# Kernel optimization log

Hardware: AMD Instinct MI355X
Metric: run time of the kernel (lower is better)

Reference implementation:

```python
import jax, jax.numpy as jnp
import numpy as np

GELU = lambda v: jax.nn.gelu(v, approximate=False)  # torch nn.GELU default (exact erf)


def _gconv(x, w):
    # grouped conv1d, valid padding; w: (C,1,K), groups=C. lax conv = cross-correlation, same as torch.
    return jax.lax.conv_general_dilated(x, w, (1,), [(0, 0)],
                                        dimension_numbers=('NCH', 'OIH', 'NCH'),
                                        feature_group_count=x.shape[1])


def _conv(x, w, b):
    # dense conv1d, kernel 3, padding=1
    y = jax.lax.conv_general_dilated(x, w, (1,), [(1, 1)],
                                     dimension_numbers=('NCH', 'OIH', 'NCH'))
    return y + b[None, :, None]


def setup_inputs() -> dict:
    key = jax.random.key(0)
    ks = jax.random.split(key, 12)
    B, C, L = 8, 64, 2048
    H, FL, HD, TD, level = 32, 8, 64, 16, 3
    Cs = (1 + level) * C  # 256 channels into the ODE
    n = lambda k, s: (jax.random.normal(k, s) * 0.05).astype(jnp.float32)
    z = lambda s: jnp.zeros(s, jnp.float32)
    return dict(
        x=jax.random.normal(ks[0], (B, C, L), jnp.float32),
        # DyWAN_QR params
        sw1=n(ks[1], (H, C)), sb1=z((H,)),
        sw2=n(ks[2], (H, H)), sb2=z((H,)),
        sw3=n(ks[3], (2 * FL, H)), sb3=z((2 * FL,)),
        # ODE time embed / FiLM params
        tw1=n(ks[4], (TD, 1)), tb1=z((TD,)),
        tw2=n(ks[5], (TD, TD)), tb2=z((TD,)),
        cw=n(ks[6], (2 * HD, TD)), cb=z((2 * HD,)),
        # ODE conv stack params
        k1=n(ks[7], (HD, Cs, 3)), kb1=z((HD,)),
        k2=n(ks[8], (HD, HD, 3)), kb2=z((HD,)),
        k3=n(ks[9], (Cs, HD, 3)), kb3=z((Cs,)),
    )


def reference(x, sw1, sb1, sw2, sb2, sw3, sb3, tw1, tb1, tw2, tb2, cw, cb,
              k1, kb1, k2, kb2, k3, kb3):
    B, C, L = x.shape
    level, FL, T = 3, 8, 5

    def dywan(a):
        # stat_net: adaptive max pool over L -> (B,C) -> Linear -> GELU
        feat = GELU(jnp.max(a, axis=-1) @ sw1.T + sb1)
        raw = GELU(feat @ sw2.T + sb2) @ sw3.T + sb3  # (B, 2*FL)
        lo_raw, hi_raw = raw[:, :FL], raw[:, FL:]
        # QR of an (FL,1) column vector == L2 normalization (up to LAPACK sign)
        lo = lo_raw / jnp.linalg.norm(lo_raw, axis=1, keepdims=True)
        hi = hi_raw / jnp.linalg.norm(hi_raw, axis=1, keepdims=True)
        return lo, hi

    pad = FL - 1
    coeffs = [x]
    approx = x
    for _ in range(level):
        lo, hi = dywan(approx)
        lo_f = jnp.broadcast_to(lo.mean(0)[None, None, :], (C, 1, FL))
        hi_f = jnp.broadcast_to(hi.mean(0)[None, None, :], (C, 1, FL))
        ap = jnp.pad(approx, ((0, 0), (0, 0), (pad // 2, pad - pad // 2)), mode='reflect')
        new_approx = _gconv(ap, lo_f)[..., :L]
        coeffs.append(_gconv(ap, hi_f)[..., :L])
        approx = new_approx
    stacked = jnp.concatenate(coeffs, axis=1)  # (B, (1+level)*C, L)

    def ode_f(t, y):
        te = jnp.reshape(t, (1, 1)).astype(y.dtype)
        te = GELU(te @ tw1.T + tb1) @ tw2.T + tb2          # (1, TD)
        cond = te @ cw.T + cb                               # (1, 2*HD)
        hd = cond.shape[1] // 2
        gamma, beta = cond[:, :hd], cond[:, hd:]
        h = _conv(y, k1, kb1)
        h = (1.0 + gamma[:, :, None]) * h + beta[:, :, None]  # FiLM
        h = GELU(h)
        h = GELU(_conv(h, k2, kb2))
        return _conv(h, k3, kb3)

    # dopri5 tableau, fixed grid over linspace(0, 1, T) (b7 = 0, so 6 stages)
    hs = 1.0 / (T - 1)
    y = stacked
    for i in range(T - 1):
        t0 = i * hs
        s1 = ode_f(t0, y)
        s2 = ode_f(t0 + hs / 5, y + hs * (1 / 5) * s1)
        s3 = ode_f(t0 + 3 * hs / 10, y + hs * (3 / 40 * s1 + 9 / 40 * s2))
        s4 = ode_f(t0 + 4 * hs / 5, y + hs * (44 / 45 * s1 - 56 / 15 * s2 + 32 / 9 * s3))
        s5 = ode_f(t0 + 8 * hs / 9, y + hs * (19372 / 6561 * s1 - 25360 / 2187 * s2
                                              + 64448 / 6561 * s3 - 212 / 729 * s4))
        s6 = ode_f(t0 + hs, y + hs * (9017 / 3168 * s1 - 355 / 33 * s2 + 46732 / 5247 * s3
                                      + 49 / 176 * s4 - 5103 / 18656 * s5))
        y = y + hs * (35 / 384 * s1 + 500 / 1113 * s3 + 125 / 192 * s4
                      - 2187 / 6784 * s5 + 11 / 84 * s6)
    ode_out = y

    yl = ode_out[:, :C, :]
    yh0 = ode_out[:, C:2 * C, :]
    yh1 = ode_out[:, 2 * C:3 * C, :]
    yh2 = ode_out[:, 3 * C:4 * C, :]

    dx = ode_f(jnp.float32(1.0), ode_out)
    inner = jnp.sum(stacked * dx, axis=(1, 2))  # (B,)
    ecloss = jnp.mean(inner ** 2)
    return (yl, yh0, yh1, yh2, ecloss)
```

## Files before the change

kernel.cpp:

```cpp
#include <hip/hip_runtime.h>
#include <math.h>

#define B 8
#define C 64
#define L 2048
#define CS 256
#define BCL  (B*C*L)
#define BCSL (B*CS*L)
#define HS 0.25f

typedef unsigned short u16;
typedef unsigned int   u32;
typedef __attribute__((ext_vector_type(8))) short sh8;
typedef __attribute__((ext_vector_type(4))) float f4;
typedef __attribute__((ext_vector_type(8))) unsigned short us8;
typedef __attribute__((ext_vector_type(4))) unsigned short us4;

__device__ __forceinline__ float gelu(float x) {
    return 0.5f * x * (1.0f + erff(x * 0.70710678118654752440f));
}
__device__ __forceinline__ u16 f2b(float f) {
    u32 u = __float_as_uint(f);
    u32 r = u + 0x7FFFu + ((u >> 16) & 1u);
    return (u16)(r >> 16);
}
__device__ __forceinline__ float b2f(u16 h) {
    return __uint_as_float(((u32)h) << 16);
}

struct ComboB { const u16* p[6]; float c[6]; };

__global__ __launch_bounds__(256) void prep_k(const float* __restrict__ w,
        u16* __restrict__ dst, int IC, int OC) {
    int idx = blockIdx.x * 256 + threadIdx.x;
    int OCG = OC >> 4;
    int j = idx & 7, lane = (idx >> 3) & 63, t = idx >> 9;
    int ocg = t % OCG, c = t / OCG;
    int oc = ocg * 16 + (lane & 15);
    int K = c * 32 + ((lane >> 4) & 3) * 8 + j;
    int kk = K / IC, ic = K % IC;
    dst[idx] = f2b(w[((size_t)oc * IC + ic) * 3 + kk]);
}

__global__ void cond25_k(const float* __restrict__ tw1, const float* __restrict__ tb1,
                         const float* __restrict__ tw2, const float* __restrict__ tb2,
                         const float* __restrict__ cw, const float* __restrict__ cb,
                         float* __restrict__ condall) {
    __shared__ float te1[16], te2[16];
    int tix = blockIdx.x;
    int tid = threadIdx.x;
    double add[6] = {0.0, 0.25/5.0, 3.0*0.25/10.0, 4.0*0.25/5.0, 8.0*0.25/9.0, 0.25};
    float t = (tix == 24) ? 1.0f : (float)((double)(tix / 6) * 0.25 + add[tix % 6]);
    if (tid < 16) te1[tid] = gelu(t * tw1[tid] + tb1[tid]);
    __syncthreads();
    if (tid < 16) {
        float s = tb2[tid];
        for (int k = 0; k < 16; ++k) s += te1[k] * tw2[tid*16+k];
        te2[tid] = s;
    }
    __syncthreads();
    float s = cb[tid];
    for (int j = 0; j < 16; ++j) s += te2[j] * cw[tid*16+j];
    condall[tix*128 + tid] = s;
}

template<int NC, int EPI>
__global__ __launch_bounds__(256) void fused_k(ComboB in,
        const u16* __restrict__ wp1, const float* __restrict__ kb1,
        const u16* __restrict__ wp2, const float* __restrict__ kb2,
        const u16* __restrict__ wp3, const float* __restrict__ kb3,
        const float* __restrict__ condall, int tix,
        u16* __restrict__ outSb,
        float* __restrict__ y, u16* __restrict__ yb,
        float* __restrict__ outp, const float* __restrict__ stacked,
        double* __restrict__ inner)
{
    __shared__ u16 xs1[50][264];
    __shared__ u16 h1t[50][72];
    __shared__ u16 h2t[34][72];
    __shared__ u16 ypart[32][264];
    __shared__ double sred[4];
    const int tid = threadIdx.x;
    const int l0  = blockIdx.x * 32;
    const int b   = blockIdx.y;
    const int g0  = l0 - 3;

    const float cy1 = HS*(35.f/384.f), cy3 = HS*(500.f/1113.f),
                cy4 = HS*(125.f/192.f), cy5 = -HS*(2187.f/6784.f),
                cy6 = HS*(11.f/84.f);

    for (int i = tid; i < 12*264; i += 256) xs1[38 + i/264][i%264] = 0;
    if (tid < 144) h1t[48 + tid/72][tid%72] = 0;

    for (int idx = tid; idx < 38*32; idx += 256) {
        int r = idx >> 5, c8 = idx & 31;
        int gl = g0 + r;
        us8 val;
        if (gl >= 0 && gl < L) {
            size_t a = ((size_t)b * L + gl) * 256 + c8 * 8;
            us8 v0 = *(const us8*)(in.p[0] + a);
            if (NC == 1) {
                val = v0;
            } else {
                float f[8];
                float yp[8];
                #pragma unroll
                for (int j = 0; j < 8; ++j) { f[j] = b2f(v0[j]); yp[j] = 0.f; }
                #pragma unroll
                for (int t = 1; t < NC; ++t) {
                    us8 vt = *(const us8*)(in.p[t] + a);
                    #pragma unroll
                    for (int j = 0; j < 8; ++j) {
                        float bv = b2f(vt[j]);
                        f[j] += in.c[t] * bv;
                        if ((EPI == 1 || EPI == 2) && (t == 1 || t == 3 || t == 4 || t == 5)) {
                            float cy = (t == 1) ? cy1 : (t == 3) ? cy3 : (t == 4) ? cy4 : cy5;
                            yp[j] += cy * bv;
                        }
                    }
                }
                #pragma unroll
                for (int j = 0; j < 8; ++j) val[j] = f2b(f[j]);
                if ((EPI == 1 || EPI == 2) && r >= 3 && r < 35) {
                    us8 ypk;
                    #pragma unroll
                    for (int j = 0; j < 8; ++j) ypk[j] = f2b(yp[j]);
                    *(us8*)&ypart[r - 3][c8 * 8] = ypk;
                }
            }
        } else {
            #pragma unroll
            for (int j = 0; j < 8; ++j) val[j] = 0;
        }
        *(us8*)&xs1[r][c8 * 8] = val;
    }
    __syncthreads();

    const int wave = tid >> 6, lane = tid & 63;
    const int nlo = lane & 15, quad = lane >> 4;

    f4 a1[3];
    a1[0] = f4{0.f,0.f,0.f,0.f}; a1[1] = a1[0]; a1[2] = a1[0];
    {
        const sh8* w1 = (const sh8*)wp1;
        for (int c = 0; c < 24; ++c) {
            int kk = c >> 3, ic0 = (c & 7) << 5;
            sh8 A = w1[(c*4 + wave)*64 + lane];
            #pragma unroll
            for (int nf = 0; nf < 3; ++nf) {
                sh8 Bv = *(const sh8*)&xs1[nf*16 + nlo + kk][ic0 + quad*8];
                a1[nf] = __builtin_amdgcn_mfma_f32_16x16x32_bf16(A, Bv, a1[nf], 0, 0, 0);
            }
        }
    }
    {
        const float* cd = condall + tix*128;
        #pragma unroll
        for (int nf = 0; nf < 3; ++nf) {
            int p = nf*16 + nlo;
            int gp = l0 - 2 + p;
            bool ok = (p < 36) && (gp >= 0) && (gp < L);
            #pragma unroll
            for (int reg = 0; reg < 4; ++reg) {
                int oc = wave*16 + quad*4 + reg;
                float v = (1.f + cd[oc]) * (a1[nf][reg] + kb1[oc]) + cd[64+oc];
                h1t[p][oc] = ok ? f2b(gelu(v)) : (u16)0;
            }
        }
    }
    __syncthreads();

    f4 a2[3];
    a2[0] = f4{0.f,0.f,0.f,0.f}; a2[1] = a2[0]; a2[2] = a2[0];
    {
        const sh8* w2 = (const sh8*)wp2;
        #pragma unroll
        for (int c = 0; c < 6; ++c) {
            int kk = c >> 1, ic0 = (c & 1) << 5;
            sh8 A = w2[(c*4 + wave)*64 + lane];
            #pragma unroll
            for (int nf = 0; nf < 3; ++nf) {
                sh8 Bv = *(const sh8*)&h1t[nf*16 + nlo + kk][ic0 + quad*8];
                a2[nf] = __builtin_amdgcn_mfma_f32_16x16x32_bf16(A, Bv, a2[nf], 0, 0, 0);
            }
        }
    }
    {
        #pragma unroll
        for (int nf = 0; nf < 3; ++nf) {
            int q = nf*16 + nlo;
            if (q < 34) {
                int gq = l0 - 1 + q;
                bool ok = (gq >= 0) && (gq < L);
                #pragma unroll
                for (int reg = 0; reg < 4; ++reg) {
                    int oc = wave*16 + quad*4 + reg;
                    h2t[q][oc] = ok ? f2b(gelu(a2[nf][reg] + kb2[oc])) : (u16)0;
                }
            }
        }
    }
    __syncthreads();

    f4 a3[4][2];
    #pragma unroll
    for (int mf = 0; mf < 4; ++mf) { a3[mf][0] = f4{0.f,0.f,0.f,0.f}; a3[mf][1] = a3[mf][0]; }
    {
        const sh8* w3 = (const sh8*)wp3;
        #pragma unroll
        for (int c = 0; c < 6; ++c) {
            int kk = c >> 1, ic0 = (c & 1) << 5;
            sh8 B0 = *(const sh8*)&h2t[nlo + kk][ic0 + quad*8];
            sh8 B1 = *(const sh8*)&h2t[16 + nlo + kk][ic0 + quad*8];
            #pragma unroll
            for (int mf = 0; mf < 4; ++mf) {
                sh8 A = w3[(c*16 + wave*4 + mf)*64 + lane];
                a3[mf][0] = __builtin_amdgcn_mfma_f32_16x16x32_bf16(A, B0, a3[mf][0], 0, 0, 0);
                a3[mf][1] = __builtin_amdgcn_mfma_f32_16x16x32_bf16(A, B1, a3[mf][1], 0, 0, 0);
            }
        }
    }

    if (EPI == 3) {
        double acc = 0.0;
        #pragma unroll
        for (int mf = 0; mf < 4; ++mf)
            #pragma unroll
            for (int nf = 0; nf < 2; ++nf) {
                int pos = l0 + nf*16 + nlo;
                #pragma unroll
                for (int reg = 0; reg < 4; ++reg) {
                    int oc = (wave*4 + mf)*16 + quad*4 + reg;
                    size_t idx = ((size_t)b*CS + oc)*L + pos;
                    float dx = a3[mf][nf][reg] + kb3[oc];
                    acc += (double)stacked[idx] * (double)dx;
                }
            }
        #pragma unroll
        for (int off = 32; off > 0; off >>= 1) acc += __shfl_down(acc, off, 64);
        if (lane == 0) sred[wave] = acc;
        __syncthreads();
        if (tid == 0) atomicAdd(&inner[b], sred[0] + sred[1] + sred[2] + sred[3]);
    } else if (EPI == 0) {
        #pragma unroll
        for (int mf = 0; mf < 4; ++mf) {
            int baseoc = (wave*4 + mf)*16 + quad*4;
            #pragma unroll
            for (int nf = 0; nf < 2; ++nf) {
                int pos = l0 + nf*16 + nlo;
                us4 pk;
                #pragma unroll
                for (int reg = 0; reg < 4; ++reg)
                    pk[reg] = f2b(a3[mf][nf][reg] + kb3[baseoc + reg]);
                *(us4*)(outSb + ((size_t)b*L + pos)*256 + baseoc) = pk;
            }
        }
    } else {
        #pragma unroll
        for (int mf = 0; mf < 4; ++mf) {
            int baseoc = (wave*4 + mf)*16 + quad*4;
            #pragma unroll
            for (int nf = 0; nf < 2; ++nf) {
                int pl = nf*16 + nlo;
                int pos = l0 + pl;
                us4 yp4 = *(const us4*)&ypart[pl][baseoc];
                us4 pk;
                #pragma unroll
                for (int reg = 0; reg < 4; ++reg) {
                    int oc = baseoc + reg;
                    size_t idx = ((size_t)b*CS + oc)*L + pos;
                    float s6 = a3[mf][nf][reg] + kb3[oc];
                    float yv = y[idx] + b2f(yp4[reg]) + cy6 * s6;
                    pk[reg] = f2b(yv);
                    if (EPI == 1) y[idx] = yv;
                    if (EPI == 2) {
                        size_t oidx = (((size_t)(oc >> 6)*B + b)*64 + (oc & 63))*L + pos;
                        outp[oidx] = yv;
                    }
                }
                *(us4*)(yb + ((size_t)b*L + pos)*256 + baseoc) = pk;
            }
        }
    }
}

__global__ __launch_bounds__(256) void rowmax_k(const float* __restrict__ a, float* __restrict__ bm) {
    __shared__ float red[256];
    int row = blockIdx.x;
    const float* p = a + (size_t)row * L;
    float m = -1e30f;
    for (int t = threadIdx.x; t < L; t += 256) m = fmaxf(m, p[t]);
    red[threadIdx.x] = m;
    __syncthreads();
    for (int s = 128; s > 0; s >>= 1) {
        if (threadIdx.x < s) red[threadIdx.x] = fmaxf(red[threadIdx.x], red[threadIdx.x + s]);
        __syncthreads();
    }
    if (threadIdx.x == 0) bm[row] = red[0];
}

__global__ __launch_bounds__(256) void mlp_k(const float* __restrict__ bm,
    const float* __restrict__ sw1, const float* __restrict__ sb1,
    const float* __restrict__ sw2, const float* __restrict__ sb2,
    const float* __restrict__ sw3, const float* __restrict__ sb3,
    float* __restrict__ filt) {
    __shared__ float m[8][64], f1[8][32], f2[8][32], raw[8][16], nrm[8][2];
    int tid = threadIdx.x;
    for (int i = tid; i < 512; i += 256) m[i >> 6][i & 63] = bm[i];
    __syncthreads();
    {
        int b = tid >> 5, h = tid & 31;
        float s = sb1[h];
        for (int c = 0; c < 64; ++c) s += m[b][c] * sw1[h*64+c];
        f1[b][h] = gelu(s);
    }
    __syncthreads();
    {
        int b = tid >> 5, h = tid & 31;
        float s = sb2[h];
        for (int k = 0; k < 32; ++k) s += f1[b][k] * sw2[h*32+k];
        f2[b][h] = gelu(s);
    }
    __syncthreads();
    if (tid < 128) {
        int b = tid >> 4, j = tid & 15;
        float s = sb3[j];
        for (int k = 0; k < 32; ++k) s += f2[b][k] * sw3[j*32+k];
        raw[b][j] = s;
    }
    __syncthreads();
    if (tid < 16) {
        int b = tid >> 1, half = tid & 1;
        float s = 0.f;
        for (int j = 0; j < 8; ++j) { float v = raw[b][half*8+j]; s += v*v; }
        nrm[b][half] = sqrtf(s);
    }
    __syncthreads();
    if (tid < 16) {
        int half = tid >> 3;
        float s = 0.f;
        for (int b = 0; b < 8; ++b) s += raw[b][tid] / nrm[b][half];
        filt[tid] = s * 0.125f;
    }
}

__global__ __launch_bounds__(256) void wconv_k(const float* __restrict__ ap,
    const float* __restrict__ filt, float* __restrict__ apOut,
    float* __restrict__ stacked, int lev) {
    __shared__ float f[16];
    if (threadIdx.x < 16) f[threadIdx.x] = filt[threadIdx.x];
    __syncthreads();
    size_t idx = (size_t)blockIdx.x * 256 + threadIdx.x;
    int l = (int)(idx & 2047);
    size_t bc = idx >> 11;
    int c = (int)(bc & 63), b = (int)(bc >> 6);
    const float* row = ap + (bc << 11);
    float lo = 0.f, hi = 0.f;
    #pragma unroll
    for (int k = 0; k < 8; ++k) {
        int mI = l + k - 3;
        mI = mI < 0 ? -mI : (mI >= L ? 2*L - 2 - mI : mI);
        float v = row[mI];
        lo += v * f[k];
        hi += v * f[8+k];
    }
    apOut[idx] = lo;
    stacked[((size_t)b * CS + (size_t)(lev+1) * 64 + c) * L + l] = hi;
}

__global__ __launch_bounds__(256) void copyx_k(const float* __restrict__ x, float* __restrict__ st) {
    size_t i = (size_t)blockIdx.x * 256 + threadIdx.x;
    size_t b = i >> 17, rem = i & 131071;
    st[b * ((size_t)CS*L) + rem] = x[i];
}

__global__ __launch_bounds__(256) void tinit_k(const float* __restrict__ st,
        float* __restrict__ y, u16* __restrict__ yb) {
    __shared__ float t[64][65];
    const int tid = threadIdx.x;
    const int l0 = blockIdx.x * 64, c0 = blockIdx.y * 64, b = blockIdx.z;
    #pragma unroll
    for (int k = 0; k < 16; ++k) {
        int c = k * 4 + (tid >> 6), l = tid & 63;
        size_t idx = ((size_t)b*CS + c0 + c) * L + l0 + l;
        float v = st[idx];
        y[idx] = v;
        t[c][l] = v;
    }
    __syncthreads();
    #pragma unroll
    for (int k = 0; k < 16; ++k) {
        int p = k * 4 + (tid >> 6), ch = tid & 63;
        yb[((size_t)b * L + l0 + p) * 256 + c0 + ch] = f2b(t[ch][p]);
    }
}

__global__ void ecfin_k(const double* __restrict__ inner, float* __restrict__ out) {
    double s = 0.0;
    for (int b = 0; b < 8; ++b) s += inner[b] * inner[b];
    out[BCSL] = (float)(s / 8.0);
}

extern "C" void kernel_launch(void* const* d_in, const int* in_sizes, int n_in,
                              void* d_out, int out_size, void* d_ws, size_t ws_size,
                              hipStream_t stream) {
    const float* x   = (const float*)d_in[0];
    const float* sw1 = (const float*)d_in[1];
    const float* sb1 = (const float*)d_in[2];
    const float* sw2 = (const float*)d_in[3];
    const float* sb2 = (const float*)d_in[4];
    const float* sw3 = (const float*)d_in[5];
    const float* sb3 = (const float*)d_in[6];
    const float* tw1 = (const float*)d_in[7];
    const float* tb1 = (const float*)d_in[8];
    const float* tw2 = (const float*)d_in[9];
    const float* tb2 = (const float*)d_in[10];
    const float* cw  = (const float*)d_in[11];
    const float* cb  = (const float*)d_in[12];
    const float* k1  = (const float*)d_in[13];
    const float* kb1 = (const float*)d_in[14];
    const float* k2  = (const float*)d_in[15];
    const float* kb2 = (const float*)d_in[16];
    const float* k3  = (const float*)d_in[17];
    const float* kb3 = (const float*)d_in[18];
    float* out = (float*)d_out;

    char* cur = (char*)d_ws;
    auto alloc = [&](size_t bytes) { void* p = cur; cur += (bytes + 255) & ~(size_t)255; return p; };
    float* stacked = (float*)alloc(BCSL * 4);
    float* y       = (float*)alloc(BCSL * 4);
    u16*   yb      = (u16*)  alloc(BCSL * 2);
    u16*   sbuf[5];
    for (int i = 0; i < 5; ++i) sbuf[i] = (u16*)alloc(BCSL * 2);
    float* cond  = (float*)alloc(3200 * 4);
    float* bmax  = (float*)alloc(512 * 4);
    float* filt  = (float*)alloc(16 * 4);
    double* inner = (double*)alloc(8 * 8);
    u16* wp1 = (u16*)alloc(49152 * 2);
    u16* wp2 = (u16*)alloc(12288 * 2);
    u16* wp3 = (u16*)alloc(49152 * 2);

    u16 *s1b = sbuf[0], *s2b = sbuf[1], *s3b = sbuf[2], *s4b = sbuf[3], *s5b = sbuf[4];

    hipMemsetAsync(inner, 0, 8 * sizeof(double), stream);

    prep_k<<<192, 256, 0, stream>>>(k1, wp1, CS, C);
    prep_k<<<48,  256, 0, stream>>>(k2, wp2, C,  C);
    prep_k<<<192, 256, 0, stream>>>(k3, wp3, C,  CS);
    cond25_k<<<25, 128, 0, stream>>>(tw1, tb1, tw2, tb2, cw, cb, cond);

    copyx_k<<<4096, 256, 0, stream>>>(x, stacked);
    const float* apIn = x;
    float* apBuf[2] = {(float*)s1b, (float*)s2b};
    for (int lev = 0; lev < 3; ++lev) {
        rowmax_k<<<512, 256, 0, stream>>>(apIn, bmax);
        mlp_k<<<1, 256, 0, stream>>>(bmax, sw1, sb1, sw2, sb2, sw3, sb3, filt);
        float* apOut = apBuf[lev & 1];
        wconv_k<<<4096, 256, 0, stream>>>(apIn, filt, apOut, stacked, lev);
        apIn = apOut;
    }
    tinit_k<<<dim3(32, 4, 8), 256, 0, stream>>>(stacked, y, yb);

    const float hs = HS;
    dim3 cg(64, 8);
    #define LAUNCH(NC, EPI, CIN, TIX, OUTSB, OUTP, STK) \
        fused_k<NC, EPI><<<cg, 256, 0, stream>>>(CIN, wp1, kb1, wp2, kb2, wp3, kb3, \
            cond, TIX, OUTSB, y, yb, OUTP, STK, inner)

    for (int i = 0; i < 4; ++i) {
        ComboB cA{}; cA.p[0] = yb;
        LAUNCH(1, 0, cA, i*6+0, s1b, nullptr, nullptr);

        ComboB cB{}; cB.p[0] = yb; cB.p[1] = s1b; cB.c[1] = hs*(1.f/5.f);
        LAUNCH(2, 0, cB, i*6+1, s2b, nullptr, nullptr);

        ComboB cC{}; cC.p[0] = yb;
        cC.p[1] = s1b; cC.c[1] = hs*(3.f/40.f);
        cC.p[2] = s2b; cC.c[2] = hs*(9.f/40.f);
        LAUNCH(3, 0, cC, i*6+2, s3b, nullptr, nullptr);

        ComboB cD{}; cD.p[0] = yb;
        cD.p[1] = s1b; cD.c[1] = hs*(44.f/45.f);
        cD.p[2] = s2b; cD.c[2] = -hs*(56.f/15.f);
        cD.p[3] = s3b; cD.c[3] = hs*(32.f/9.f);
        LAUNCH(4, 0, cD, i*6+3, s4b, nullptr, nullptr);

        ComboB cE{}; cE.p[0] = yb;
        cE.p[1] = s1b; cE.c[1] = hs*(19372.f/6561.f);
        cE.p[2] = s2b; cE.c[2] = -hs*(25360.f/2187.f);
        cE.p[3] = s3b; cE.c[3] = hs*(64448.f/6561.f);
        cE.p[4] = s4b; cE.c[4] = -hs*(212.f/729.f);
        LAUNCH(5, 0, cE, i*6+4, s5b, nullptr, nullptr);

        ComboB cF{}; cF.p[0] = yb;
        cF.p[1] = s1b; cF.c[1] = hs*(9017.f/3168.f);
        cF.p[2] = s2b; cF.c[2] = -hs*(355.f/33.f);
        cF.p[3] = s3b; cF.c[3] = hs*(46732.f/5247.f);
        cF.p[4] = s4b; cF.c[4] = hs*(49.f/176.f);
        cF.p[5] = s5b; cF.c[5] = -hs*(5103.f/18656.f);
        if (i < 3) {
            LAUNCH(6, 1, cF, i*6+5, nullptr, nullptr, nullptr);
        } else {
            LAUNCH(6, 2, cF, i*6+5, nullptr, out, nullptr);
        }
    }

    ComboB cZ{}; cZ.p[0] = yb;
    LAUNCH(1, 3, cZ, 24, nullptr, nullptr, stacked);
    ecfin_k<<<1, 1, 0, stream>>>(inner, out);
    #undef LAUNCH
}
```

Measured before the change: 689.7 us.

## Use 512-thread fused ODE blocks and fold row-max into producer kernels

The fused conv-stack kernel now runs 8 waves per block instead of 4. The work is split so that stages 1-2 divide the N fragments across wave halves and stage 3 divides the output-channel fragments, which gives each wave fewer accumulators and more parallelism per block. The h1/h2 stores are packed into 4-wide writes. Separately, the per-level row-max reductions move into copyx_k and wconv_k using order-preserving atomicMax encodings, which removes three rowmax launches and their extra read of the activations. The cost is more block-level reductions and atomics, and the 2-of-3 N-fragment split leaves the upper four waves partly idle in stages 1 and 2.

```diff
diff --git a/kernel.cpp b/kernel.cpp
--- a/kernel.cpp
+++ b/kernel.cpp
@@ -26,6 +26,13 @@
 }
 __device__ __forceinline__ float b2f(u16 h) {
     return __uint_as_float(((u32)h) << 16);
+}
+__device__ __forceinline__ u32 encmax(float f) {
+    u32 b = __float_as_uint(f);
+    return (b & 0x80000000u) ? ~b : (b | 0x80000000u);
+}
+__device__ __forceinline__ float decmax(u32 u) {
+    return __uint_as_float((u & 0x80000000u) ? (u ^ 0x80000000u) : ~u);
 }
 
 struct ComboB { const u16* p[6]; float c[6]; };
@@ -65,7 +72,7 @@
 }
 
 template<int NC, int EPI>
-__global__ __launch_bounds__(256) void fused_k(ComboB in,
+__global__ __launch_bounds__(512) void fused_k(ComboB in,
         const u16* __restrict__ wp1, const float* __restrict__ kb1,
         const u16* __restrict__ wp2, const float* __restrict__ kb2,
         const u16* __restrict__ wp3, const float* __restrict__ kb3,
@@ -79,7 +86,7 @@
     __shared__ u16 h1t[50][72];
     __shared__ u16 h2t[34][72];
     __shared__ u16 ypart[32][264];
-    __shared__ double sred[4];
+    __shared__ double sred[8];
     const int tid = threadIdx.x;
     const int l0  = blockIdx.x * 32;
     const int b   = blockIdx.y;
@@ -89,10 +96,10 @@
                 cy4 = HS*(125.f/192.f), cy5 = -HS*(2187.f/6784.f),
                 cy6 = HS*(11.f/84.f);
 
-    for (int i = tid; i < 12*264; i += 256) xs1[38 + i/264][i%264] = 0;
+    for (int i = tid; i < 12*264; i += 512) xs1[38 + i/264][i%264] = 0;
     if (tid < 144) h1t[48 + tid/72][tid%72] = 0;
 
-    for (int idx = tid; idx < 38*32; idx += 256) {
+    for (int idx = tid; idx < 38*32; idx += 512) {
         int r = idx >> 5, c8 = idx & 31;
         int gl = g0 + r;
         us8 val;
@@ -139,72 +146,92 @@
     const int wave = tid >> 6, lane = tid & 63;
     const int nlo = lane & 15, quad = lane >> 4;
 
-    f4 a1[3];
-    a1[0] = f4{0.f,0.f,0.f,0.f}; a1[1] = a1[0]; a1[2] = a1[0];
+    const int ocg12  = wave & 3;
+    const int nfbase = (wave < 4) ? 0 : 2;
+    const int nfcnt  = (wave < 4) ? 2 : 1;
+
+    f4 a1[2];
+    a1[0] = f4{0.f,0.f,0.f,0.f}; a1[1] = a1[0];
     {
         const sh8* w1 = (const sh8*)wp1;
         for (int c = 0; c < 24; ++c) {
             int kk = c >> 3, ic0 = (c & 7) << 5;
-            sh8 A = w1[(c*4 + wave)*64 + lane];
-            #pragma unroll
-            for (int nf = 0; nf < 3; ++nf) {
-                sh8 Bv = *(const sh8*)&xs1[nf*16 + nlo + kk][ic0 + quad*8];
-                a1[nf] = __builtin_amdgcn_mfma_f32_16x16x32_bf16(A, Bv, a1[nf], 0, 0, 0);
+            sh8 A = w1[(c*4 + ocg12)*64 + lane];
+            #pragma unroll
+            for (int k = 0; k < 2; ++k) {
+                if (k < nfcnt) {
+                    int nf = nfbase + k;
+                    sh8 Bv = *(const sh8*)&xs1[nf*16 + nlo + kk][ic0 + quad*8];
+                    a1[k] = __builtin_amdgcn_mfma_f32_16x16x32_bf16(A, Bv, a1[k], 0, 0, 0);
+                }
             }
         }
     }
     {
         const float* cd = condall + tix*128;
-        #pragma unroll
-        for (int nf = 0; nf < 3; ++nf) {
-            int p = nf*16 + nlo;
-            int gp = l0 - 2 + p;
-            bool ok = (p < 36) && (gp >= 0) && (gp < L);
-            #pragma unroll
-            for (int reg = 0; reg < 4; ++reg) {
-                int oc = wave*16 + quad*4 + reg;
-                float v = (1.f + cd[oc]) * (a1[nf][reg] + kb1[oc]) + cd[64+oc];
-                h1t[p][oc] = ok ? f2b(gelu(v)) : (u16)0;
-            }
-        }
-    }
-    __syncthreads();
-
-    f4 a2[3];
-    a2[0] = f4{0.f,0.f,0.f,0.f}; a2[1] = a2[0]; a2[2] = a2[0];
+        const int oc0 = ocg12*16 + quad*4;
+        #pragma unroll
+        for (int k = 0; k < 2; ++k) {
+            if (k < nfcnt) {
+                int nf = nfbase + k;
+                int p = nf*16 + nlo;
+                int gp = l0 - 2 + p;
+                bool ok = (p < 36) && (gp >= 0) && (gp < L);
+                us4 pk;
+                #pragma unroll
+                for (int reg = 0; reg < 4; ++reg) {
+                    int oc = oc0 + reg;
+                    float v = (1.f + cd[oc]) * (a1[k][reg] + kb1[oc]) + cd[64+oc];
+                    pk[reg] = ok ? f2b(gelu(v)) : (u16)0;
+                }
+                *(us4*)&h1t[p][oc0] = pk;
+            }
+        }
+    }
+    __syncthreads();
+
+    f4 a2[2];
+    a2[0] = f4{0.f,0.f,0.f,0.f}; a2[1] = a2[0];
     {
         const sh8* w2 = (const sh8*)wp2;
         #pragma unroll
         for (int c = 0; c < 6; ++c) {
             int kk = c >> 1, ic0 = (c & 1) << 5;
-            sh8 A = w2[(c*4 + wave)*64 + lane];
-            #pragma unroll
-            for (int nf = 0; nf < 3; ++nf) {
-                sh8 Bv = *(const sh8*)&h1t[nf*16 + nlo + kk][ic0 + quad*8];
-                a2[nf] = __builtin_amdgcn_mfma_f32_16x16x32_bf16(A, Bv, a2[nf], 0, 0, 0);
-            }
-        }
-    }
-    {
-        #pragma unroll
-        for (int nf = 0; nf < 3; ++nf) {
-            int q = nf*16 + nlo;
-            if (q < 34) {
-                int gq = l0 - 1 + q;
-                bool ok = (gq >= 0) && (gq < L);
-                #pragma unroll
-                for (int reg = 0; reg < 4; ++reg) {
-                    int oc = wave*16 + quad*4 + reg;
-                    h2t[q][oc] = ok ? f2b(gelu(a2[nf][reg] + kb2[oc])) : (u16)0;
-                }
-            }
-        }
-    }
-    __syncthreads();
-
-    f4 a3[4][2];
+            sh8 A = w2[(c*4 + ocg12)*64 + lane];
+            #pragma unroll
+            for (int k = 0; k < 2; ++k) {
+                if (k < nfcnt) {
+                    int nf = nfbase + k;
+                    sh8 Bv = *(const sh8*)&h1t[nf*16 + nlo + kk][ic0 + quad*8];
+                    a2[k] = __builtin_amdgcn_mfma_f32_16x16x32_bf16(A, Bv, a2[k], 0, 0, 0);
+                }
+            }
+        }
+    }
+    {
+        const int oc0 = ocg12*16 + quad*4;
+        #pragma unroll
+        for (int k = 0; k < 2; ++k) {
+            if (k < nfcnt) {
+                int nf = nfbase + k;
+                int q = nf*16 + nlo;
+                if (q < 34) {
+                    int gq = l0 - 1 + q;
+                    bool ok = (gq >= 0) && (gq < L);
+                    us4 pk;
+                    #pragma unroll
+                    for (int reg = 0; reg < 4; ++reg)
+                        pk[reg] = ok ? f2b(gelu(a2[k][reg] + kb2[oc0 + reg])) : (u16)0;
+                    *(us4*)&h2t[q][oc0] = pk;
+                }
+            }
+        }
+    }
+    __syncthreads();
+
+    f4 a3[2][2];
     #pragma unroll
-    for (int mf = 0; mf < 4; ++mf) { a3[mf][0] = f4{0.f,0.f,0.f,0.f}; a3[mf][1] = a3[mf][0]; }
+    for (int mf = 0; mf < 2; ++mf) { a3[mf][0] = f4{0.f,0.f,0.f,0.f}; a3[mf][1] = a3[mf][0]; }
     {
         const sh8* w3 = (const sh8*)wp3;
         #pragma unroll
@@ -213,8 +240,8 @@
             sh8 B0 = *(const sh8*)&h2t[nlo + kk][ic0 + quad*8];
             sh8 B1 = *(const sh8*)&h2t[16 + nlo + kk][ic0 + quad*8];
             #pragma unroll
-            for (int mf = 0; mf < 4; ++mf) {
-                sh8 A = w3[(c*16 + wave*4 + mf)*64 + lane];
+            for (int mf = 0; mf < 2; ++mf) {
+                sh8 A = w3[(c*16 + wave*2 + mf)*64 + lane];
                 a3[mf][0] = __builtin_amdgcn_mfma_f32_16x16x32_bf16(A, B0, a3[mf][0], 0, 0, 0);
                 a3[mf][1] = __builtin_amdgcn_mfma_f32_16x16x32_bf16(A, B1, a3[mf][1], 0, 0, 0);
             }
@@ -224,13 +251,13 @@
     if (EPI == 3) {
         double acc = 0.0;
         #pragma unroll
-        for (int mf = 0; mf < 4; ++mf)
+        for (int mf = 0; mf < 2; ++mf)
             #pragma unroll
             for (int nf = 0; nf < 2; ++nf) {
                 int pos = l0 + nf*16 + nlo;
                 #pragma unroll
                 for (int reg = 0; reg < 4; ++reg) {
-                    int oc = (wave*4 + mf)*16 + quad*4 + reg;
+                    int oc = (wave*2 + mf)*16 + quad*4 + reg;
                     size_t idx = ((size_t)b*CS + oc)*L + pos;
                     float dx = a3[mf][nf][reg] + kb3[oc];
                     acc += (double)stacked[idx] * (double)dx;
@@ -240,11 +267,16 @@
         for (int off = 32; off > 0; off >>= 1) acc += __shfl_down(acc, off, 64);
         if (lane == 0) sred[wave] = acc;
         __syncthreads();
-        if (tid == 0) atomicAdd(&inner[b], sred[0] + sred[1] + sred[2] + sred[3]);
+        if (tid == 0) {
+            double s = 0.0;
+            #pragma unroll
+            for (int w = 0; w < 8; ++w) s += sred[w];
+            atomicAdd(&inner[b], s);
+        }
     } else if (EPI == 0) {
         #pragma unroll
-        for (int mf = 0; mf < 4; ++mf) {
-            int baseoc = (wave*4 + mf)*16 + quad*4;
+        for (int mf = 0; mf < 2; ++mf) {
+            int baseoc = (wave*2 + mf)*16 + quad*4;
             #pragma unroll
             for (int nf = 0; nf < 2; ++nf) {
                 int pos = l0 + nf*16 + nlo;
@@ -257,8 +289,8 @@
         }
     } else {
         #pragma unroll
-        for (int mf = 0; mf < 4; ++mf) {
-            int baseoc = (wave*4 + mf)*16 + quad*4;
+        for (int mf = 0; mf < 2; ++mf) {
+            int baseoc = (wave*2 + mf)*16 + quad*4;
             #pragma unroll
             for (int nf = 0; nf < 2; ++nf) {
                 int pl = nf*16 + nlo;
@@ -284,29 +316,14 @@
     }
 }
 
-__global__ __launch_bounds__(256) void rowmax_k(const float* __restrict__ a, float* __restrict__ bm) {
-    __shared__ float red[256];
-    int row = blockIdx.x;
-    const float* p = a + (size_t)row * L;
-    float m = -1e30f;
-    for (int t = threadIdx.x; t < L; t += 256) m = fmaxf(m, p[t]);
-    red[threadIdx.x] = m;
-    __syncthreads();
-    for (int s = 128; s > 0; s >>= 1) {
-        if (threadIdx.x < s) red[threadIdx.x] = fmaxf(red[threadIdx.x], red[threadIdx.x + s]);
-        __syncthreads();
-    }
-    if (threadIdx.x == 0) bm[row] = red[0];
-}
-
-__global__ __launch_bounds__(256) void mlp_k(const float* __restrict__ bm,
+__global__ __launch_bounds__(256) void mlp_k(const u32* __restrict__ bm,
     const float* __restrict__ sw1, const float* __restrict__ sb1,
     const float* __restrict__ sw2, const float* __restrict__ sb2,
     const float* __restrict__ sw3, const float* __restrict__ sb3,
     float* __restrict__ filt) {
     __shared__ float m[8][64], f1[8][32], f2[8][32], raw[8][16], nrm[8][2];
     int tid = threadIdx.x;
-    for (int i = tid; i < 512; i += 256) m[i >> 6][i & 63] = bm[i];
+    for (int i = tid; i < 512; i += 256) m[i >> 6][i & 63] = decmax(bm[i]);
     __syncthreads();
     {
         int b = tid >> 5, h = tid & 31;
@@ -346,8 +363,9 @@
 
 __global__ __launch_bounds__(256) void wconv_k(const float* __restrict__ ap,
     const float* __restrict__ filt, float* __restrict__ apOut,
-    float* __restrict__ stacked, int lev) {
+    float* __restrict__ stacked, int lev, u32* __restrict__ bmaxn) {
     __shared__ float f[16];
+    __shared__ float red[256];
     if (threadIdx.x < 16) f[threadIdx.x] = filt[threadIdx.x];
     __syncthreads();
     size_t idx = (size_t)blockIdx.x * 256 + threadIdx.x;
@@ -364,14 +382,33 @@
         lo += v * f[k];
         hi += v * f[8+k];
     }
-    apOut[idx] = lo;
     stacked[((size_t)b * CS + (size_t)(lev+1) * 64 + c) * L + l] = hi;
-}
-
-__global__ __launch_bounds__(256) void copyx_k(const float* __restrict__ x, float* __restrict__ st) {
+    if (bmaxn) {
+        apOut[idx] = lo;
+        red[threadIdx.x] = lo;
+        __syncthreads();
+        for (int s = 128; s > 0; s >>= 1) {
+            if (threadIdx.x < s) red[threadIdx.x] = fmaxf(red[threadIdx.x], red[threadIdx.x + s]);
+            __syncthreads();
+        }
+        if (threadIdx.x == 0) atomicMax(&bmaxn[blockIdx.x >> 3], encmax(red[0]));
+    }
+}
+
+__global__ __launch_bounds__(256) void copyx_k(const float* __restrict__ x,
+        float* __restrict__ st, u32* __restrict__ bmax0) {
+    __shared__ float red[256];
     size_t i = (size_t)blockIdx.x * 256 + threadIdx.x;
     size_t b = i >> 17, rem = i & 131071;
-    st[b * ((size_t)CS*L) + rem] = x[i];
+    float v = x[i];
+    st[b * ((size_t)CS*L) + rem] = v;
+    red[threadIdx.x] = v;
+    __syncthreads();
+    for (int s = 128; s > 0; s >>= 1) {
+        if (threadIdx.x < s) red[threadIdx.x] = fmaxf(red[threadIdx.x], red[threadIdx.x + s]);
+        __syncthreads();
+    }
+    if (threadIdx.x == 0) atomicMax(&bmax0[blockIdx.x >> 3], encmax(red[0]));
 }
 
 __global__ __launch_bounds__(256) void tinit_k(const float* __restrict__ st,
@@ -433,30 +470,30 @@
     u16*   sbuf[5];
     for (int i = 0; i < 5; ++i) sbuf[i] = (u16*)alloc(BCSL * 2);
     float* cond  = (float*)alloc(3200 * 4);
-    float* bmax  = (float*)alloc(512 * 4);
+    double* inner = (double*)alloc(8 * 8);
+    u32* bmaxe   = (u32*)alloc(3 * 512 * 4);
     float* filt  = (float*)alloc(16 * 4);
-    double* inner = (double*)alloc(8 * 8);
     u16* wp1 = (u16*)alloc(49152 * 2);
     u16* wp2 = (u16*)alloc(12288 * 2);
     u16* wp3 = (u16*)alloc(49152 * 2);
 
     u16 *s1b = sbuf[0], *s2b = sbuf[1], *s3b = sbuf[2], *s4b = sbuf[3], *s5b = sbuf[4];
 
-    hipMemsetAsync(inner, 0, 8 * sizeof(double), stream);
+    hipMemsetAsync(inner, 0, 256 + 3 * 512 * 4, stream);
 
     prep_k<<<192, 256, 0, stream>>>(k1, wp1, CS, C);
     prep_k<<<48,  256, 0, stream>>>(k2, wp2, C,  C);
     prep_k<<<192, 256, 0, stream>>>(k3, wp3, C,  CS);
     cond25_k<<<25, 128, 0, stream>>>(tw1, tb1, tw2, tb2, cw, cb, cond);
 
-    copyx_k<<<4096, 256, 0, stream>>>(x, stacked);
+    copyx_k<<<4096, 256, 0, stream>>>(x, stacked, bmaxe);
     const float* apIn = x;
     float* apBuf[2] = {(float*)s1b, (float*)s2b};
     for (int lev = 0; lev < 3; ++lev) {
-        rowmax_k<<<512, 256, 0, stream>>>(apIn, bmax);
-        mlp_k<<<1, 256, 0, stream>>>(bmax, sw1, sb1, sw2, sb2, sw3, sb3, filt);
+        mlp_k<<<1, 256, 0, stream>>>(bmaxe + lev*512, sw1, sb1, sw2, sb2, sw3, sb3, filt);
         float* apOut = apBuf[lev & 1];
-        wconv_k<<<4096, 256, 0, stream>>>(apIn, filt, apOut, stacked, lev);
+        wconv_k<<<4096, 256, 0, stream>>>(apIn, filt, apOut, stacked, lev,
+                                          (lev < 2) ? (bmaxe + (lev+1)*512) : nullptr);
         apIn = apOut;
     }
     tinit_k<<<dim3(32, 4, 8), 256, 0, stream>>>(stacked, y, yb);
@@ -464,7 +501,7 @@
     const float hs = HS;
     dim3 cg(64, 8);
     #define LAUNCH(NC, EPI, CIN, TIX, OUTSB, OUTP, STK) \
-        fused_k<NC, EPI><<<cg, 256, 0, stream>>>(CIN, wp1, kb1, wp2, kb2, wp3, kb3, \
+        fused_k<NC, EPI><<<cg, 512, 0, stream>>>(CIN, wp1, kb1, wp2, kb2, wp3, kb3, \
             cond, TIX, OUTSB, y, yb, OUTP, STK, inner)
 
     for (int i = 0; i < 4; ++i) {
```

New measurement: 696.0 us. About the same (+0.9%).
